# Performance work log

Measured on AMD Instinct MI355X. Metric: run time of the kernel, lower is better.

## Reference

```python
import jax, jax.numpy as jnp
import numpy as np

NUM_FEAT = 1024
NUM_GROUP = 16
DIM_K = NUM_FEAT // NUM_GROUP  # 64
FEAT_DIM = 64
WAVE_LENGTH = 1000.0


def position_embedding(box, ctx_box):
    # box: (M,4), ctx_box: (N,4) corner encoding -> (M*N, 64)
    xmin, ymin, xmax, ymax = jnp.split(box, 4, axis=1)            # (M,1) each
    bw = xmax - xmin + 1.0
    bh = ymax - ymin + 1.0
    cx = 0.5 * (xmin + xmax)
    cy = 0.5 * (ymin + ymax)
    cxmin, cymin, cxmax, cymax = jnp.split(ctx_box, 4, axis=1)    # (N,1) each
    cbw = cxmax - cxmin + 1.0
    cbh = cymax - cymin + 1.0
    ccx = 0.5 * (cxmin + cxmax)
    ccy = 0.5 * (cymin + cymax)
    dx = jnp.log(jnp.clip(jnp.abs((cx - ccx.T) / bw), 1e-3))      # (M,N)
    dy = jnp.log(jnp.clip(jnp.abs((cy - ccy.T) / bh), 1e-3))
    dw = jnp.log(cbw.T / bw)
    dh = jnp.log(cbh.T / bh)
    pos = jnp.stack((dx, dy, dw, dh), axis=2)                     # (M,N,4)
    feat_range = jnp.arange(FEAT_DIM // 8, dtype=jnp.float32)     # (8,)
    dim_mat = jnp.power(jnp.float32(WAVE_LENGTH), (8.0 / FEAT_DIM) * feat_range)
    div = (100.0 * pos)[..., None] / dim_mat                      # (M,N,4,8)
    emb = jnp.concatenate((jnp.sin(div), jnp.cos(div)), axis=3)   # (M,N,4,16)
    M, N = pos.shape[0], pos.shape[1]
    return emb.reshape(M * N, FEAT_DIM)


def setup_inputs() -> dict:
    key = jax.random.key(0)
    ks = jax.random.split(key, 12)
    M, N = 512, 1024

    def make_boxes(k, n):
        k1, k2 = jax.random.split(k)
        xy = jax.random.uniform(k1, (n, 2), dtype=jnp.float32) * 800.0
        wh = jax.random.uniform(k2, (n, 2), dtype=jnp.float32) * 200.0 + 1.0
        return jnp.concatenate([xy, xy + wh], axis=1)             # valid corners

    return {
        "feat": jax.random.normal(ks[0], (M, NUM_FEAT), dtype=jnp.float32),
        "ctx_feat": jax.random.normal(ks[1], (N, NUM_FEAT), dtype=jnp.float32),
        "box": make_boxes(ks[2], M),
        "ctx_box": make_boxes(ks[3], N),
        # torch Linear stores weight as (out, in); apply as x @ W.T + b
        "w_fc_gt": jax.random.normal(ks[4], (NUM_FEAT, 1024), dtype=jnp.float32) * 0.01,
        "b_fc_gt": jnp.zeros((NUM_FEAT,), dtype=jnp.float32),
        "w_fc_ctx": jax.random.normal(ks[5], (NUM_FEAT, 1024), dtype=jnp.float32) * 0.01,
        "b_fc_ctx": jnp.zeros((NUM_FEAT,), dtype=jnp.float32),
        "w_pos_gt": jax.random.normal(ks[6], (NUM_GROUP, FEAT_DIM), dtype=jnp.float32) * 0.01,
        "b_pos_gt": jnp.zeros((NUM_GROUP,), dtype=jnp.float32),
        "w_pos_ctx": jax.random.normal(ks[7], (NUM_GROUP, FEAT_DIM), dtype=jnp.float32) * 0.01,
        "b_pos_ctx": jnp.zeros((NUM_GROUP,), dtype=jnp.float32),
        # grouped 1x1 conv (16384 -> 1024, groups=16): per-group weight (64 out, 1024 in)
        "w_conv": jax.random.normal(ks[8], (NUM_GROUP, DIM_K, NUM_FEAT), dtype=jnp.float32) * 0.02,
        "b_conv": jnp.zeros((NUM_FEAT,), dtype=jnp.float32),
    }


def reference(feat, ctx_feat, box, ctx_box,
              w_fc_gt, b_fc_gt, w_fc_ctx, b_fc_ctx,
              w_pos_gt, b_pos_gt, w_pos_ctx, b_pos_ctx,
              w_conv, b_conv):
    M, N = feat.shape[0], ctx_feat.shape[0]
    # positional bias per group: (M*N,64) -relu-> linear -> (G,M,N)
    pe_gt = jax.nn.relu(position_embedding(box, ctx_box))
    pos_gt = (pe_gt @ w_pos_gt.T + b_pos_gt).T.reshape(NUM_GROUP, M, N)
    pe_ctx = jax.nn.relu(position_embedding(ctx_box, box))
    pos_ctx = (pe_ctx @ w_pos_ctx.T + b_pos_ctx).T.reshape(NUM_GROUP, N, M)
    # grouped projections
    q = (feat @ w_fc_gt.T + b_fc_gt).reshape(M, NUM_GROUP, DIM_K)
    k = (ctx_feat @ w_fc_ctx.T + b_fc_ctx).reshape(N, NUM_GROUP, DIM_K)
    scores = jnp.einsum('mgd,ngd->gmn', q, k) / np.float32(np.sqrt(DIM_K))  # (G,M,N)
    # gt <- ctx attention with log-position bias
    w1 = jax.nn.softmax(jnp.log(jnp.clip(pos_gt, 1e-6)) + scores, axis=-1)  # (G,M,N)
    att1 = jnp.einsum('gmn,nc->mgc', w1, ctx_feat)                          # (M,G,1024)
    out_gt = jnp.einsum('mgc,goc->mgo', att1, w_conv).reshape(M, NUM_FEAT) + b_conv
    # ctx <- gt attention (note: original module reuses gt_ctx_linear_out here)
    w2 = jax.nn.softmax(jnp.log(jnp.clip(pos_ctx, 1e-6)) + scores.transpose(0, 2, 1), axis=-1)  # (G,N,M)
    att2 = jnp.einsum('gnm,mc->ngc', w2, feat)                              # (N,G,1024)
    out_ctx = jnp.einsum('ngc,goc->ngo', att2, w_conv).reshape(N, NUM_FEAT) + b_conv
    return out_gt, out_ctx
```

## Files before the change

### kernel.cpp

```cpp
#include <hip/hip_runtime.h>
#include <math.h>


typedef __attribute__((ext_vector_type(8))) short short8;
typedef __attribute__((ext_vector_type(4))) float floatx4;
typedef __attribute__((ext_vector_type(4))) _Float16 half4;
typedef __attribute__((ext_vector_type(4))) unsigned uint4v;

__device__ inline unsigned short f32_bf16_rne(float x) {
    union { float f; unsigned u; } v; v.f = x;
    unsigned u = v.u;
    return (unsigned short)((u + 0x7fffu + ((u >> 16) & 1u)) >> 16);
}

__device__ inline unsigned fbits(float x) {
    union { float f; unsigned u; } v; v.f = x; return v.u;
}
__device__ inline float bitsf(unsigned u) {
    union { unsigned u; float f; } v; v.u = u; return v.f;
}
__device__ inline float h16f(unsigned short u) {
    union { unsigned short u; _Float16 h; } v; v.u = u; return (float)v.h;
}

__device__ __forceinline__ floatx4 mfma16(short8 a, short8 b, floatx4 c) {
    return __builtin_amdgcn_mfma_f32_16x16x32_bf16(a, b, c, 0, 0, 0);
}

__device__ __forceinline__ void gemm_tile_pack(
    const unsigned short* __restrict__ Ab, int lda,
    const unsigned short* __restrict__ Bb, int ldb, int K,
    unsigned short* __restrict__ out_base,
    const float* __restrict__ biasvec,
    unsigned short* As, unsigned short* Bs)
{
    const int tid = threadIdx.x;
    const int lr = tid >> 3;
    const int lk = (tid & 7) * 8;
    const int lane = tid & 63;
    const int wave = tid >> 6;
    const int qr = (wave >> 1) * 32;
    const int qc = (wave & 1) * 32;
    const int m = lane & 15;
    const int quad = lane >> 4;

    const unsigned short* Ap  = Ab + (long long)lr * lda + lk;
    const unsigned short* Ap2 = Ap + 32LL * lda;
    const unsigned short* Bp  = Bb + (long long)lr * ldb + lk;
    const unsigned short* Bp2 = Bp + 32LL * ldb;
    unsigned short* AsW  = As + lr * 72 + lk;
    unsigned short* AsW2 = As + (lr + 32) * 72 + lk;
    unsigned short* BsW  = Bs + lr * 72 + lk;
    unsigned short* BsW2 = Bs + (lr + 32) * 72 + lk;
    const unsigned short* a0p = As + (qr + m) * 72 + quad * 8;
    const unsigned short* b0p = Bs + (qc + m) * 72 + quad * 8;

    floatx4 acc00 = {0.f,0.f,0.f,0.f}, acc01 = {0.f,0.f,0.f,0.f};
    floatx4 acc10 = {0.f,0.f,0.f,0.f}, acc11 = {0.f,0.f,0.f,0.f};

    int4 pa0 = *(const int4*)Ap;
    int4 pa1 = *(const int4*)Ap2;
    int4 pb0 = *(const int4*)Bp;
    int4 pb1 = *(const int4*)Bp2;
    int4 qa0 = *(const int4*)(Ap + 64);
    int4 qa1 = *(const int4*)(Ap2 + 64);
    int4 qb0 = *(const int4*)(Bp + 64);
    int4 qb1 = *(const int4*)(Bp2 + 64);

    for (int k0 = 0; ; ) {
        __syncthreads();
        *(int4*)AsW  = pa0;
        *(int4*)AsW2 = pa1;
        *(int4*)BsW  = pb0;
        *(int4*)BsW2 = pb1;
        __syncthreads();
        pa0 = qa0; pa1 = qa1; pb0 = qb0; pb1 = qb1;
        const int kf = k0 + 128;
        if (kf < K) {
            qa0 = *(const int4*)(Ap + kf);
            qa1 = *(const int4*)(Ap2 + kf);
            qb0 = *(const int4*)(Bp + kf);
            qb1 = *(const int4*)(Bp2 + kf);
        }
        #pragma unroll
        for (int kk = 0; kk < 64; kk += 32) {
            short8 a0 = *(const short8*)(a0p + kk);
            short8 a1 = *(const short8*)(a0p + 16 * 72 + kk);
            short8 b0 = *(const short8*)(b0p + kk);
            short8 b1 = *(const short8*)(b0p + 16 * 72 + kk);
            acc00 = mfma16(a0, b0, acc00);
            acc01 = mfma16(a0, b1, acc01);
            acc10 = mfma16(a1, b0, acc10);
            acc11 = mfma16(a1, b1, acc11);
        }
        k0 += 64;
        if (k0 >= K) break;
    }

    float bias0 = 0.f, bias1 = 0.f;
    if (biasvec) { bias0 = biasvec[qc + m]; bias1 = biasvec[qc + 16 + m]; }

    __syncthreads();
    const floatx4 accs[2][2] = { {acc00, acc01}, {acc10, acc11} };
    #pragma unroll
    for (int i = 0; i < 2; ++i)
        #pragma unroll
        for (int r = 0; r < 4; ++r) {
            const int lrow = qr + i * 16 + quad * 4 + r;
            #pragma unroll
            for (int j = 0; j < 2; ++j) {
                const int lcol = qc + j * 16 + m;
                float val = accs[i][j][r] + (j ? bias1 : bias0);
                As[lrow * 72 + lcol] = f32_bf16_rne(val);
            }
        }
    __syncthreads();
    #pragma unroll
    for (int h = 0; h < 2; ++h) {
        const int f = h * 2048 + tid * 8;
        const int lanep = (f >> 3) & 63;
        const int part = (f >> 9) & 1;
        const int ploc = f >> 10;
        const int row = ploc * 16 + (lanep & 15);
        const int col = part * 32 + ((lanep >> 4) << 3);
        short8 v8 = *(const short8*)&As[row * 72 + col];
        *(short8*)(out_base + f) = v8;
    }
}

__global__ __launch_bounds__(256) void cast_kernel(
    const float* __restrict__ s0, unsigned short* __restrict__ d0,
    const float* __restrict__ s1, unsigned short* __restrict__ d1,
    const float* __restrict__ s2, unsigned short* __restrict__ d2,
    const float* __restrict__ s3, unsigned short* __restrict__ d3,
    const float* __restrict__ s4, unsigned short* __restrict__ d4)
{
    int bc = blockIdx.x;
    const float* s; unsigned short* d;
    if (bc < 512)       { s = s0; d = d0; }
    else if (bc < 1536) { s = s1; d = d1; bc -= 512; }
    else if (bc < 2560) { s = s2; d = d2; bc -= 1536; }
    else if (bc < 3584) { s = s3; d = d3; bc -= 2560; }
    else                { s = s4; d = d4; bc -= 3584; }
    const int idx = (bc * 256 + threadIdx.x) * 4;
    float4 v = *(const float4*)(s + idx);
    ushort4 o;
    o.x = f32_bf16_rne(v.x); o.y = f32_bf16_rne(v.y);
    o.z = f32_bf16_rne(v.z); o.w = f32_bf16_rne(v.w);
    *(ushort4*)(d + idx) = o;
}

__global__ __launch_bounds__(256) void posproj_kernel(
    const float* __restrict__ box, const float* __restrict__ ctx_box,
    const float* __restrict__ w_gt, const float* __restrict__ b_gt,
    const float* __restrict__ w_ctx, const float* __restrict__ b_ctx,
    _Float16* __restrict__ bias_gt, _Float16* __restrict__ bias_ctx,
    const unsigned short* __restrict__ in_bf, const unsigned short* __restrict__ wgt,
    const unsigned short* __restrict__ wctx,
    const float* __restrict__ bgt, const float* __restrict__ bctx,
    unsigned short* __restrict__ qk_pack,
    const unsigned short* __restrict__ wconv, unsigned short* __restrict__ vt_pack)
{
    __shared__ __align__(16) unsigned short smem[64 * 72 * 2];
    const int i = blockIdx.x;

    int pi;
    if (i < 4608) {
        const int k48 = i / 48;
        const int r48 = i - k48 * 48;
        if (r48 < 8) {
            const int j = r48;
            const int k = k48;
            const int g = j + 8 * (k & 1);
            const int rest = k >> 1;
            const int z = rest / 24;
            const int cc = rest - z * 24;
            unsigned short* As = smem;
            unsigned short* Bs = smem + 64 * 72;
            if (z == 0) {
                const int bm = cc * 64;
                const unsigned short* B = (bm < 512) ? wgt : wctx;
                const float* bias = (bm < 512) ? bgt : bctx;
                gemm_tile_pack(in_bf + (long long)bm * 1024, 1024,
                               B + (long long)g * 65536, 1024, 1024,
                               qk_pack + ((long long)g * 96 + cc * 4) * 1024,
                               bias + g * 64, As, Bs);
            } else {
                gemm_tile_pack(wconv + (long long)g * 65536, 1024,
                               in_bf + (long long)cc * 65536, 1024, 1024,
                               vt_pack + ((long long)g * 24 + cc) * 4096,
                               nullptr, As, Bs);
            }
            return;
        }
        pi = i - k48 * 8 - 8;
    } else {
        pi = i - 768;
    }

    const bool first = (pi < 2048);
    const long long blk = first ? pi : (pi - 2048);
    const float* boxA = first ? box : ctx_box;
    const float* boxB = first ? ctx_box : box;
    const float* w_pos = first ? w_gt : w_ctx;
    const float* b_pos = first ? b_gt : b_ctx;
    _Float16* out = first ? bias_gt : bias_ctx;
    const int shift = first ? 10 : 9;

    const int tid = threadIdx.x;
    const int lane = tid & 63;
    const int w = tid >> 6;
    const int m = lane & 15;
    const int quad = lane >> 4;
    const bool qlow = (quad < 2);
    const float phase = (quad & 1) ? 1.57079632679f : 0.0f;
    const float bpv = b_pos[m];
    const int plB = w * 16 + m;

    union { uint4v u; short8 s; } bH0, bH1, bL0, bL1;
    {
        const float* wrow = w_pos + m * 64 + quad * 8;
        unsigned h0[4], h1[4], l0[4], l1[4];
        #pragma unroll
        for (int t = 0; t < 4; ++t) {
            float2 w0 = *(const float2*)(wrow + 2 * t);
            float2 w1 = *(const float2*)(wrow + 32 + 2 * t);
            unsigned u0 = fbits(w0.x), u1 = fbits(w0.y);
            unsigned v0 = fbits(w1.x), v1 = fbits(w1.y);
            unsigned r0 = fbits(w0.x - bitsf(u0 & 0xFFFF0000u));
            unsigned r1 = fbits(w0.y - bitsf(u1 & 0xFFFF0000u));
            unsigned s0 = fbits(w1.x - bitsf(v0 & 0xFFFF0000u));
            unsigned s1 = fbits(w1.y - bitsf(v1 & 0xFFFF0000u));
            h0[t] = (u0 >> 16) | (u1 & 0xFFFF0000u);
            h1[t] = (v0 >> 16) | (v1 & 0xFFFF0000u);
            l0[t] = (r0 >> 16) | (r1 & 0xFFFF0000u);
            l1[t] = (s0 >> 16) | (s1 & 0xFFFF0000u);
        }
        bH0.u = (uint4v){h0[0], h0[1], h0[2], h0[3]};
        bH1.u = (uint4v){h1[0], h1[1], h1[2], h1[3]};
        bL0.u = (uint4v){l0[0], l0[1], l0[2], l0[3]};
        bL1.u = (uint4v){l1[0], l1[1], l1[2], l1[3]};
    }

    const float w100[8] = {100.f, 42.169650342f, 17.782794100f, 7.498942093f,
                           3.162277660f, 1.333521432f, 0.562341325f, 0.237137371f};
    const long long pbase = blk * 256;

    for (int it = 0; it < 4; ++it) {
        const long long pb = pbase + it * 64;

        const int i2 = (int)(pb >> shift);
        const int j2 = (int)(pb & ((1 << shift) - 1)) + plB;
        float4 ba = *(const float4*)(boxA + i2 * 4);
        float4 bb = *(const float4*)(boxB + j2 * 4);
        const float a0 = qlow ? ba.x : ba.y, a1 = qlow ? ba.z : ba.w;
        const float b0 = qlow ? bb.x : bb.y, b1 = qlow ? bb.z : bb.w;
        const float rr = __builtin_amdgcn_rcpf(a1 - a0 + 1.f);
        const float pos_lo =
            __logf(fmaxf(fabsf((0.5f*(a0+a1) - 0.5f*(b0+b1)) * rr), 1e-3f));
        const float pos_hi = __logf((b1 - b0 + 1.f) * rr);

        unsigned hp0[4], lp0[4], hp1[4], lp1[4];
        #pragma unroll
        for (int fi = 0; fi < 4; ++fi) {
            float x0 = fmaxf(__sinf(fmaf(w100[2*fi],     pos_lo, phase)), 0.f);
            float x1 = fmaxf(__sinf(fmaf(w100[2*fi + 1], pos_lo, phase)), 0.f);
            unsigned u0 = fbits(x0), u1 = fbits(x1);
            unsigned r0 = fbits(x0 - bitsf(u0 & 0xFFFF0000u));
            unsigned r1 = fbits(x1 - bitsf(u1 & 0xFFFF0000u));
            hp0[fi] = (u0 >> 16) | (u1 & 0xFFFF0000u);
            lp0[fi] = (r0 >> 16) | (r1 & 0xFFFF0000u);
            float y0 = fmaxf(__sinf(fmaf(w100[2*fi],     pos_hi, phase)), 0.f);
            float y1 = fmaxf(__sinf(fmaf(w100[2*fi + 1], pos_hi, phase)), 0.f);
            unsigned v0 = fbits(y0), v1 = fbits(y1);
            unsigned s0r = fbits(y0 - bitsf(v0 & 0xFFFF0000u));
            unsigned s1r = fbits(y1 - bitsf(v1 & 0xFFFF0000u));
            hp1[fi] = (v0 >> 16) | (v1 & 0xFFFF0000u);
            lp1[fi] = (s0r >> 16) | (s1r & 0xFFFF0000u);
        }
        union { uint4v u; short8 s; } cH0, cL0, cH1, cL1;
        cH0.u = (uint4v){hp0[0], hp0[1], hp0[2], hp0[3]};
        cL0.u = (uint4v){lp0[0], lp0[1], lp0[2], lp0[3]};
        cH1.u = (uint4v){hp1[0], hp1[1], hp1[2], hp1[3]};
        cL1.u = (uint4v){lp1[0], lp1[1], lp1[2], lp1[3]};

        floatx4 acc = {0.f, 0.f, 0.f, 0.f};
        acc = mfma16(cH0.s, bH0.s, acc);
        acc = mfma16(cH1.s, bH1.s, acc);
        acc = mfma16(cH0.s, bL0.s, acc);
        acc = mfma16(cH1.s, bL1.s, acc);
        acc = mfma16(cL0.s, bH0.s, acc);
        acc = mfma16(cL1.s, bH1.s, acc);

        half4 hv;
        #pragma unroll
        for (int r = 0; r < 4; ++r)
            hv[r] = (_Float16)fmaxf(acc[r] + bpv, 1e-6f);
        *(half4*)(out + (long long)m * 524288 + pb + w * 16 + quad * 4) = hv;
    }
}

template <int NC>
__device__ __forceinline__ void attn_body(
    int g, int bm,
    const unsigned short* __restrict__ qk, int pA0, int pB0,
    const _Float16* __restrict__ bias,
    const unsigned short* __restrict__ vt, int cc0,
    const float* __restrict__ b_conv, float* __restrict__ outp,
    unsigned short* wpack, float* redB)
{
    constexpr int NCOL = NC * 64;
    constexpr int WS = NCOL + 8;
    constexpr int SHIFT = (NC == 16) ? 10 : 9;
    constexpr int NSTG = (32 * NCOL) / (512 * 8);

    const int tid = threadIdx.x;
    const int lane = tid & 63;
    const int w = tid >> 6;
    const int ws = w >> 2;
    const int wq = w & 3;
    const int m = lane & 15;
    const int quad = lane >> 4;

    {
        const _Float16* bsrc = bias + (long long)g * 524288 + (long long)bm * NCOL;
        _Float16* bb = (_Float16*)wpack;
        #pragma unroll
        for (int i = 0; i < NSTG; ++i) {
            const int idx = (i * 512 + tid) * 8;
            const int row = idx >> SHIFT;
            const int col = idx & (NCOL - 1);
            *(int4*)(bb + row * WS + col) = *(const int4*)(bsrc + idx);
        }
    }

    const unsigned short* abase = qk + ((long long)(g * 96 + pA0 + ws)) * 1024;
    short8 aq0 = *(const short8*)(abase + lane * 8);
    short8 aq1 = *(const short8*)(abase + 512 + lane * 8);

    const unsigned short* bptr = qk + ((long long)(g * 96 + pB0 + wq)) * 1024 + lane * 8;
    short8 B0[2], B1[2];
    B0[0] = *(const short8*)bptr;
    B1[0] = *(const short8*)(bptr + 512);
    B0[1] = *(const short8*)(bptr + 4096);
    B1[1] = *(const short8*)(bptr + 4096 + 512);

    __syncthreads();

    const int slot0 = (ws * 16 + quad * 4) * WS + wq * 16 + m;
    float rsum[4] = {0.f, 0.f, 0.f, 0.f};
    #pragma unroll
    for (int c = 0; c < NC; ++c) {
        floatx4 acc = {0.f, 0.f, 0.f, 0.f};
        acc = mfma16(aq0, B0[c & 1], acc);
        acc = mfma16(aq1, B1[c & 1], acc);
        if (c + 2 < NC) {
            const unsigned short* nb = bptr + (long long)(c + 2) * 4096;
            B0[c & 1] = *(const short8*)nb;
            B1[c & 1] = *(const short8*)(nb + 512);
        }
        #pragma unroll
        for (int r = 0; r < 4; ++r) {
            const int a = slot0 + r * WS + c * 64;
            float p = h16f(wpack[a]);
            float e = exp2f(acc[r] * 0.18033688f) * p;
            rsum[r] += e;
            wpack[a] = f32_bf16_rne(e);
        }
    }

    const unsigned short* vptr = vt + ((long long)(g * 24 + cc0)) * 4096
                               + wq * 1024 + lane * 8;
    short8 V0[2], V1[2];
    V0[0] = *(const short8*)vptr;
    V1[0] = *(const short8*)(vptr + 512);
    V0[1] = *(const short8*)(vptr + 4096);
    V1[1] = *(const short8*)(vptr + 4096 + 512);

    #pragma unroll
    for (int r = 0; r < 4; ++r)
        #pragma unroll
        for (int off = 1; off < 16; off <<= 1)
            rsum[r] += __shfl_xor(rsum[r], off, 64);
    if (m == 0) {
        #pragma unroll
        for (int r = 0; r < 4; ++r) redB[w * 16 + quad * 4 + r] = rsum[r];
    }
    __syncthreads();

    float rinv[4];
    #pragma unroll
    for (int r = 0; r < 4; ++r)
        rinv[r] = 1.f / (redB[ws*64 + quad*4+r] + redB[ws*64 + 16 + quad*4+r] +
                         redB[ws*64 + 32 + quad*4+r] + redB[ws*64 + 48 + quad*4+r]);

    floatx4 oacc = {0.f, 0.f, 0.f, 0.f};
    const unsigned short* awp = wpack + (ws * 16 + m) * WS + quad * 8;
    #pragma unroll
    for (int kc = 0; kc < NC; ++kc) {
        short8 a0 = *(const short8*)(awp + kc * 64);
        short8 a1 = *(const short8*)(awp + kc * 64 + 32);
        oacc = mfma16(a0, V0[kc & 1], oacc);
        oacc = mfma16(a1, V1[kc & 1], oacc);
        if (kc + 2 < NC) {
            const unsigned short* nv = vptr + (long long)(kc + 2) * 4096;
            V0[kc & 1] = *(const short8*)nv;
            V1[kc & 1] = *(const short8*)(nv + 512);
        }
    }

    const int o = wq * 16 + m;
    const float bc = b_conv[g * 64 + o];
    __syncthreads();
    float* ot = (float*)wpack;
    #pragma unroll
    for (int r = 0; r < 4; ++r)
        ot[(ws * 16 + quad * 4 + r) * 68 + o] = fmaf(oacc[r], rinv[r], bc);
    __syncthreads();
    const int orow = tid >> 4, oc4 = (tid & 15) * 4;
    float4 ov = *(const float4*)&ot[orow * 68 + oc4];
    *(float4*)(outp + (long long)(bm + orow) * 1024 + g * 64 + oc4) = ov;
}

__global__ __launch_bounds__(512) void attn_out_kernel(
    const unsigned short* __restrict__ qk_pack,
    const _Float16* __restrict__ bias_gt, const _Float16* __restrict__ bias_ctx,
    const unsigned short* __restrict__ vt_pack, const float* __restrict__ b_conv,
    float* __restrict__ out_gt, float* __restrict__ out_ctx)
{
    __shared__ __align__(16) unsigned short wpack[32 * 1032];
    __shared__ float redB[128];

    const int bx = blockIdx.x;
    if (bx < 256) {
        const int g = bx & 15;
        const int rb = bx >> 4;
        attn_body<16>(g, rb * 32, qk_pack, 2 * rb, 32,
                      bias_gt, vt_pack, 8, b_conv, out_gt,
                      wpack, redB);
    } else {
        const int b2 = bx - 256;
        const int g = b2 & 15;
        const int rb = b2 >> 4;
        attn_body<8>(g, rb * 32, qk_pack, 32 + 2 * rb, 0,
                     bias_ctx, vt_pack, 0, b_conv, out_ctx,
                     wpack, redB);
    }
}

extern "C" void kernel_launch(void* const* d_in, const int* in_sizes, int n_in,
                              void* d_out, int out_size, void* d_ws, size_t ws_size,
                              hipStream_t stream)
{
    const float* feat     = (const float*)d_in[0];
    const float* ctx_feat = (const float*)d_in[1];
    const float* box      = (const float*)d_in[2];
    const float* ctx_box  = (const float*)d_in[3];
    const float* w_fc_gt  = (const float*)d_in[4];
    const float* b_fc_gt  = (const float*)d_in[5];
    const float* w_fc_ctx = (const float*)d_in[6];
    const float* b_fc_ctx = (const float*)d_in[7];
    const float* w_pos_gt = (const float*)d_in[8];
    const float* b_pos_gt = (const float*)d_in[9];
    const float* w_pos_ctx= (const float*)d_in[10];
    const float* b_pos_ctx= (const float*)d_in[11];
    const float* w_conv   = (const float*)d_in[12];
    const float* b_conv   = (const float*)d_in[13];

    float* ws = (float*)d_ws;
    unsigned short* in_bf   = (unsigned short*)ws;
    unsigned short* ctx_bf  = in_bf + 524288LL;
    unsigned short* qk_pack = in_bf + 1572864LL;
    _Float16* bias_gt  = (_Float16*)(ws + 1572864LL);
    _Float16* bias_ctx = (_Float16*)(ws + 5767168LL);
    unsigned short* wconv_bf = (unsigned short*)(ws + 9961472LL);
    unsigned short* vt_pack  = (unsigned short*)(ws + 10485760LL);
    unsigned short* wfcgt_bf = (unsigned short*)(ws + 11272192LL);
    unsigned short* wfcctx_bf= wfcgt_bf + 1048576LL;

    float* out_gt  = (float*)d_out;
    float* out_ctx = (float*)d_out + 524288LL;

    hipLaunchKernelGGL(cast_kernel, dim3(4608), dim3(256), 0, stream,
                       feat, in_bf,
                       ctx_feat, ctx_bf,
                       w_fc_gt, wfcgt_bf,
                       w_fc_ctx, wfcctx_bf,
                       w_conv, wconv_bf);

    hipLaunchKernelGGL(posproj_kernel, dim3(4864), dim3(256), 0, stream,
                       box, ctx_box, w_pos_gt, b_pos_gt, w_pos_ctx, b_pos_ctx,
                       bias_gt, bias_ctx,
                       in_bf, wfcgt_bf, wfcctx_bf, b_fc_gt, b_fc_ctx, qk_pack,
                       wconv_bf, vt_pack);

    hipLaunchKernelGGL(attn_out_kernel, dim3(768), dim3(512), 0, stream,
                       qk_pack, bias_gt, bias_ctx, vt_pack, b_conv, out_gt, out_ctx);
}
```

Before: 148.4 us.

## Enlarge GEMM tiles to 128x128 and double posproj block size

Replaces the 64x64 bf16 GEMM tiles in the fused projection kernel with 128x128 tiles computed by 512-thread blocks. Each wave now holds a 32x64 accumulator block, which raises operand reuse from LDS and halves the number of GEMM blocks. The position-embedding blocks are also doubled in size, and the interleaving of GEMM and positional work across the grid is remapped (3 GEMM blocks per 35). The costs are larger LDS use and higher register pressure per block, which may lower occupancy.

```diff
diff --git a/kernel.cpp b/kernel.cpp
--- a/kernel.cpp
+++ b/kernel.cpp
@@ -27,36 +27,43 @@
     return __builtin_amdgcn_mfma_f32_16x16x32_bf16(a, b, c, 0, 0, 0);
 }
 
-__device__ __forceinline__ void gemm_tile_pack(
-    const unsigned short* __restrict__ Ab, int lda,
-    const unsigned short* __restrict__ Bb, int ldb, int K,
-    unsigned short* __restrict__ out_base,
+__device__ __forceinline__ void gemm128_core(
+    const unsigned short* __restrict__ Ab,
+    const unsigned short* __restrict__ Bb,
     const float* __restrict__ biasvec,
-    unsigned short* As, unsigned short* Bs)
+    unsigned short* smem)
 {
     const int tid = threadIdx.x;
+    const int lane = tid & 63;
+    const int wave = tid >> 6;
+    const int wr = wave >> 1;
+    const int wc = wave & 1;
+    const int m = lane & 15;
+    const int quad = lane >> 4;
+
+    unsigned short* As = smem;
+    unsigned short* Bs = smem + 128 * 72;
+
     const int lr = tid >> 3;
     const int lk = (tid & 7) * 8;
-    const int lane = tid & 63;
-    const int wave = tid >> 6;
-    const int qr = (wave >> 1) * 32;
-    const int qc = (wave & 1) * 32;
-    const int m = lane & 15;
-    const int quad = lane >> 4;
-
-    const unsigned short* Ap  = Ab + (long long)lr * lda + lk;
-    const unsigned short* Ap2 = Ap + 32LL * lda;
-    const unsigned short* Bp  = Bb + (long long)lr * ldb + lk;
-    const unsigned short* Bp2 = Bp + 32LL * ldb;
+
+    const unsigned short* Ap  = Ab + (long long)lr * 1024 + lk;
+    const unsigned short* Ap2 = Ap + 64LL * 1024;
+    const unsigned short* Bp  = Bb + (long long)lr * 1024 + lk;
+    const unsigned short* Bp2 = Bp + 64LL * 1024;
     unsigned short* AsW  = As + lr * 72 + lk;
-    unsigned short* AsW2 = As + (lr + 32) * 72 + lk;
+    unsigned short* AsW2 = As + (lr + 64) * 72 + lk;
     unsigned short* BsW  = Bs + lr * 72 + lk;
-    unsigned short* BsW2 = Bs + (lr + 32) * 72 + lk;
-    const unsigned short* a0p = As + (qr + m) * 72 + quad * 8;
-    const unsigned short* b0p = Bs + (qc + m) * 72 + quad * 8;
-
-    floatx4 acc00 = {0.f,0.f,0.f,0.f}, acc01 = {0.f,0.f,0.f,0.f};
-    floatx4 acc10 = {0.f,0.f,0.f,0.f}, acc11 = {0.f,0.f,0.f,0.f};
+    unsigned short* BsW2 = Bs + (lr + 64) * 72 + lk;
+    const unsigned short* a0p = As + (wr * 32 + m) * 72 + quad * 8;
+    const unsigned short* b0p = Bs + (wc * 64 + m) * 72 + quad * 8;
+
+    floatx4 acc[2][4];
+    #pragma unroll
+    for (int i = 0; i < 2; ++i)
+        #pragma unroll
+        for (int n = 0; n < 4; ++n)
+            acc[i][n] = (floatx4){0.f, 0.f, 0.f, 0.f};
 
     int4 pa0 = *(const int4*)Ap;
     int4 pa1 = *(const int4*)Ap2;
@@ -76,56 +83,49 @@
         __syncthreads();
         pa0 = qa0; pa1 = qa1; pb0 = qb0; pb1 = qb1;
         const int kf = k0 + 128;
-        if (kf < K) {
+        if (kf < 1024) {
             qa0 = *(const int4*)(Ap + kf);
             qa1 = *(const int4*)(Ap2 + kf);
             qb0 = *(const int4*)(Bp + kf);
             qb1 = *(const int4*)(Bp2 + kf);
         }
         #pragma unroll
-        for (int kk = 0; kk < 64; kk += 32) {
-            short8 a0 = *(const short8*)(a0p + kk);
-            short8 a1 = *(const short8*)(a0p + 16 * 72 + kk);
-            short8 b0 = *(const short8*)(b0p + kk);
-            short8 b1 = *(const short8*)(b0p + 16 * 72 + kk);
-            acc00 = mfma16(a0, b0, acc00);
-            acc01 = mfma16(a0, b1, acc01);
-            acc10 = mfma16(a1, b0, acc10);
-            acc11 = mfma16(a1, b1, acc11);
+        for (int ks = 0; ks < 64; ks += 32) {
+            short8 a0 = *(const short8*)(a0p + ks);
+            short8 a1 = *(const short8*)(a0p + 16 * 72 + ks);
+            short8 b0 = *(const short8*)(b0p + ks);
+            short8 b1 = *(const short8*)(b0p + 16 * 72 + ks);
+            short8 b2 = *(const short8*)(b0p + 32 * 72 + ks);
+            short8 b3 = *(const short8*)(b0p + 48 * 72 + ks);
+            acc[0][0] = mfma16(a0, b0, acc[0][0]);
+            acc[1][0] = mfma16(a1, b0, acc[1][0]);
+            acc[0][1] = mfma16(a0, b1, acc[0][1]);
+            acc[1][1] = mfma16(a1, b1, acc[1][1]);
+            acc[0][2] = mfma16(a0, b2, acc[0][2]);
+            acc[1][2] = mfma16(a1, b2, acc[1][2]);
+            acc[0][3] = mfma16(a0, b3, acc[0][3]);
+            acc[1][3] = mfma16(a1, b3, acc[1][3]);
         }
         k0 += 64;
-        if (k0 >= K) break;
-    }
-
-    float bias0 = 0.f, bias1 = 0.f;
-    if (biasvec) { bias0 = biasvec[qc + m]; bias1 = biasvec[qc + 16 + m]; }
+        if (k0 >= 1024) break;
+    }
+
+    float bv[4];
+    #pragma unroll
+    for (int n = 0; n < 4; ++n)
+        bv[n] = biasvec ? biasvec[wc * 64 + n * 16 + m] : 0.f;
 
     __syncthreads();
-    const floatx4 accs[2][2] = { {acc00, acc01}, {acc10, acc11} };
+    unsigned short* C = smem;
     #pragma unroll
     for (int i = 0; i < 2; ++i)
         #pragma unroll
-        for (int r = 0; r < 4; ++r) {
-            const int lrow = qr + i * 16 + quad * 4 + r;
+        for (int n = 0; n < 4; ++n)
             #pragma unroll
-            for (int j = 0; j < 2; ++j) {
-                const int lcol = qc + j * 16 + m;
-                float val = accs[i][j][r] + (j ? bias1 : bias0);
-                As[lrow * 72 + lcol] = f32_bf16_rne(val);
-            }
-        }
+            for (int r = 0; r < 4; ++r)
+                C[(wr * 32 + i * 16 + quad * 4 + r) * 136 + wc * 64 + n * 16 + m] =
+                    f32_bf16_rne(acc[i][n][r] + bv[n]);
     __syncthreads();
-    #pragma unroll
-    for (int h = 0; h < 2; ++h) {
-        const int f = h * 2048 + tid * 8;
-        const int lanep = (f >> 3) & 63;
-        const int part = (f >> 9) & 1;
-        const int ploc = f >> 10;
-        const int row = ploc * 16 + (lanep & 15);
-        const int col = part * 32 + ((lanep >> 4) << 3);
-        short8 v8 = *(const short8*)&As[row * 72 + col];
-        *(short8*)(out_base + f) = v8;
-    }
 }
 
 __global__ __launch_bounds__(256) void cast_kernel(
@@ -150,7 +150,7 @@
     *(ushort4*)(d + idx) = o;
 }
 
-__global__ __launch_bounds__(256) void posproj_kernel(
+__global__ __launch_bounds__(512) void posproj_kernel(
     const float* __restrict__ box, const float* __restrict__ ctx_box,
     const float* __restrict__ w_gt, const float* __restrict__ b_gt,
     const float* __restrict__ w_ctx, const float* __restrict__ b_ctx,
@@ -161,45 +161,72 @@
     unsigned short* __restrict__ qk_pack,
     const unsigned short* __restrict__ wconv, unsigned short* __restrict__ vt_pack)
 {
-    __shared__ __align__(16) unsigned short smem[64 * 72 * 2];
+    __shared__ __align__(16) unsigned short smem[128 * 72 * 2];
     const int i = blockIdx.x;
-
-    int pi;
-    if (i < 4608) {
-        const int k48 = i / 48;
-        const int r48 = i - k48 * 48;
-        if (r48 < 8) {
-            const int j = r48;
-            const int k = k48;
-            const int g = j + 8 * (k & 1);
-            const int rest = k >> 1;
-            const int z = rest / 24;
-            const int cc = rest - z * 24;
-            unsigned short* As = smem;
-            unsigned short* Bs = smem + 64 * 72;
-            if (z == 0) {
-                const int bm = cc * 64;
-                const unsigned short* B = (bm < 512) ? wgt : wctx;
-                const float* bias = (bm < 512) ? bgt : bctx;
-                gemm_tile_pack(in_bf + (long long)bm * 1024, 1024,
-                               B + (long long)g * 65536, 1024, 1024,
-                               qk_pack + ((long long)g * 96 + cc * 4) * 1024,
-                               bias + g * 64, As, Bs);
-            } else {
-                gemm_tile_pack(wconv + (long long)g * 65536, 1024,
-                               in_bf + (long long)cc * 65536, 1024, 1024,
-                               vt_pack + ((long long)g * 24 + cc) * 4096,
-                               nullptr, As, Bs);
+    const int win = i / 35;
+    const int r35 = i - win * 35;
+    const int tid = threadIdx.x;
+
+    if (r35 < 3) {
+        const int t = win * 3 + r35;
+        if (t < 96) {
+            const int rowtile = t >> 3, coltile = t & 7;
+            const int rowbase = rowtile * 128, colbase = coltile * 128;
+            const unsigned short* w = (rowtile < 4) ? wgt : wctx;
+            const float* bias = (rowtile < 4) ? bgt : bctx;
+            gemm128_core(in_bf + (long long)rowbase * 1024,
+                         w + (long long)colbase * 1024,
+                         bias + colbase, smem);
+            const unsigned short* C = smem;
+            const int gbase = coltile * 2, pbase = rowtile * 8;
+            #pragma unroll
+            for (int h = 0; h < 4; ++h) {
+                const int f = h * 4096 + tid * 8;
+                const int sub = f >> 10;
+                const int gsel = sub >> 3, p = sub & 7;
+                const int rem = f & 1023;
+                const int part = rem >> 9;
+                const int ln = (rem >> 3) & 63;
+                const int row = p * 16 + (ln & 15);
+                const int col = gsel * 64 + part * 32 + ((ln >> 4) << 3);
+                short8 v = *(const short8*)&C[row * 136 + col];
+                *(short8*)(qk_pack
+                    + ((long long)((gbase + gsel) * 96 + pbase + p)) * 1024
+                    + part * 512 + ln * 8) = v;
             }
-            return;
-        }
-        pi = i - k48 * 8 - 8;
-    } else {
-        pi = i - 768;
-    }
-
-    const bool first = (pi < 2048);
-    const long long blk = first ? pi : (pi - 2048);
+        } else {
+            const int t2 = t - 96;
+            const int rowtile = t2 & 7, coltile = t2 >> 3;
+            const int rowbase = rowtile * 128, colbase = coltile * 128;
+            gemm128_core(wconv + (long long)rowbase * 1024,
+                         in_bf + (long long)colbase * 1024,
+                         nullptr, smem);
+            const unsigned short* C = smem;
+            const int gbase = rowtile * 2, ccbase = coltile * 2;
+            #pragma unroll
+            for (int h = 0; h < 4; ++h) {
+                const int f = h * 4096 + tid * 8;
+                const int sub = f >> 10;
+                const int gsel = sub >> 3;
+                const int q = sub & 7;
+                const int ccsel = q >> 2, p = q & 3;
+                const int rem = f & 1023;
+                const int part = rem >> 9;
+                const int ln = (rem >> 3) & 63;
+                const int row = gsel * 64 + p * 16 + (ln & 15);
+                const int col = ccsel * 64 + part * 32 + ((ln >> 4) << 3);
+                short8 v = *(const short8*)&C[row * 136 + col];
+                *(short8*)(vt_pack
+                    + ((long long)((gbase + gsel) * 24 + ccbase + ccsel)) * 4096
+                    + p * 1024 + part * 512 + ln * 8) = v;
+            }
+        }
+        return;
+    }
+
+    const int pi = win * 32 + (r35 - 3);
+    const bool first = (pi < 1024);
+    const long long blk = first ? pi : (pi - 1024);
     const float* boxA = first ? box : ctx_box;
     const float* boxB = first ? ctx_box : box;
     const float* w_pos = first ? w_gt : w_ctx;
@@ -207,7 +234,6 @@
     _Float16* out = first ? bias_gt : bias_ctx;
     const int shift = first ? 10 : 9;
 
-    const int tid = threadIdx.x;
     const int lane = tid & 63;
     const int w = tid >> 6;
     const int m = lane & 15;
@@ -244,10 +270,10 @@
 
     const float w100[8] = {100.f, 42.169650342f, 17.782794100f, 7.498942093f,
                            3.162277660f, 1.333521432f, 0.562341325f, 0.237137371f};
-    const long long pbase = blk * 256;
+    const long long pbase = blk * 512;
 
     for (int it = 0; it < 4; ++it) {
-        const long long pb = pbase + it * 64;
+        const long long pb = pbase + it * 128;
 
         const int i2 = (int)(pb >> shift);
         const int j2 = (int)(pb & ((1 << shift) - 1)) + plB;
@@ -488,7 +514,7 @@
                        w_fc_ctx, wfcctx_bf,
                        w_conv, wconv_bf);
 
-    hipLaunchKernelGGL(posproj_kernel, dim3(4864), dim3(256), 0, stream,
+    hipLaunchKernelGGL(posproj_kernel, dim3(2240), dim3(512), 0, stream,
                        box, ctx_box, w_pos_gt, b_pos_gt, w_pos_ctx, b_pos_ctx,
                        bias_gt, bias_ctx,
                        in_bf, wfcgt_bf, wfcctx_bf, b_fc_gt, b_fc_ctx, qk_pack,
```

New measurement: 157.0 us. 5.8% more time.
